# Optimization experiments

Hardware: AMD Instinct MI355X
Metric: run time of the kernel (lower is better)

## Reference

```python
import jax, jax.numpy as jnp
import numpy as np

N_NODES = 50000
N_EDGES = 1600000
HIDDEN = 128
IN_DIM = 3  # x (1) + relative pos (2)


def setup_inputs() -> dict:
    key = jax.random.key(0)
    ks = jax.random.split(key, 5)
    x = jax.random.normal(ks[0], (N_NODES, 1), dtype=jnp.float32)
    pos = jax.random.normal(ks[1], (N_NODES, 2), dtype=jnp.float32)
    # MLP params (Linear(3,128) -> ReLU -> Linear(128,128)), fan-in scaled
    W1 = jax.random.normal(ks[2], (IN_DIM, HIDDEN), dtype=jnp.float32) / np.sqrt(IN_DIM)
    b1 = jnp.zeros((HIDDEN,), dtype=jnp.float32)
    W2 = jax.random.normal(ks[3], (HIDDEN, HIDDEN), dtype=jnp.float32) / np.sqrt(HIDDEN)
    b2 = jnp.zeros((HIDDEN,), dtype=jnp.float32)
    edge_index = jax.random.randint(ks[4], (2, N_EDGES), 0, N_NODES, dtype=jnp.int64)
    return {"x": x, "pos": pos, "W1": W1, "b1": b1, "W2": W2, "b2": b2,
            "edge_index": edge_index}


def reference(x, pos, W1, b1, W2, b2, edge_index):
    # PTConv with aggr='add': per-edge message = nn(cat([x_j, pos_j - pos_i]))
    # then scatter-add into destination node i.
    src = edge_index[0]  # j (neighbor / source)
    dst = edge_index[1]  # i (center / destination)
    msg_in = jnp.concatenate([x[src], pos[src] - pos[dst]], axis=-1)  # [E, 3]
    h = jax.nn.relu(msg_in @ W1 + b1) @ W2 + b2                        # [E, 128]
    out = jax.ops.segment_sum(h, dst, num_segments=x.shape[0])        # [N, 128]
    return out
```

## Files before the change

### kernel.cpp

```cpp
#include <hip/hip_runtime.h>


#define HIDDEN 128
#define BNODES 16
#define BSH 4
#define SUPSH 10
#define CAPA 36864
#define CAPF 768
#define EPBA 1024
#define KSUB 16
#define SThrB 512
#define W2LD 136

typedef float v2f __attribute__((ext_vector_type(2)));
typedef short bf16x8 __attribute__((ext_vector_type(8)));
typedef float f32x4 __attribute__((ext_vector_type(4)));

__device__ __forceinline__ unsigned cvt_pk_bf16(float lo, float hi) {
    unsigned r;
    asm("v_cvt_pk_bf16_f32 %0, %1, %2" : "=v"(r) : "v"(lo), "v"(hi));
    return r;
}

__device__ __forceinline__ unsigned short f2bf(float f) {
    unsigned int u = __float_as_uint(f);
    u += 0x7fffu + ((u >> 16) & 1u);
    return (unsigned short)(u >> 16);
}

__global__ __launch_bounds__(256) void k_histA(const int* __restrict__ dst,
                                               const float* __restrict__ x,
                                               const float* __restrict__ pos,
                                               const float* __restrict__ W2,
                                               int* __restrict__ histA,
                                               float4* __restrict__ xpos,
                                               unsigned short* __restrict__ w2bfT,
                                               int E, int N, int NBLK) {
    __shared__ int h[64];
    int tid = threadIdx.x;
    if (tid < 64) h[tid] = 0;
    int nb = blockIdx.x * 64 + tid;
    if (tid < 64 && nb < N) {
        float2 p = ((const float2*)pos)[nb];
        xpos[nb] = make_float4(x[nb], p.x, p.y, 0.f);
    }
    if (blockIdx.x == gridDim.x - 1) {
        for (int idx = tid; idx < HIDDEN * HIDDEN; idx += 256) {
            int k = idx >> 7, c = idx & 127;
            w2bfT[c * HIDDEN + k] = f2bf(W2[idx]);
        }
    }
    __syncthreads();
    int base = blockIdx.x * EPBA;
    int lim = base + EPBA; if (lim > E) lim = E;
    if (base < lim) {
        int n = lim - base;
        int n4 = ((E & 3) == 0) ? (n >> 2) : 0;
        const int4* d4 = (const int4*)(dst + base);
        for (int i = tid; i < n4; i += 256) {
            int4 d = d4[i];
            atomicAdd(&h[d.x >> SUPSH], 1);
            atomicAdd(&h[d.y >> SUPSH], 1);
            atomicAdd(&h[d.z >> SUPSH], 1);
            atomicAdd(&h[d.w >> SUPSH], 1);
        }
        for (int i = base + (n4 << 2) + tid; i < lim; i += 256)
            atomicAdd(&h[dst[i] >> SUPSH], 1);
    }
    __syncthreads();
    if (tid < 64 && blockIdx.x < NBLK) histA[tid * NBLK + blockIdx.x] = h[tid];
}

__global__ __launch_bounds__(256) void k_scanA(int* __restrict__ histA,
                                               int* __restrict__ bcurA, int NBLK) {
    __shared__ int sums[256];
    int s = blockIdx.x;
    int tid = threadIdx.x;
    int* col = histA + (size_t)s * NBLK;
    int per = (NBLK + 255) >> 8;
    int b0 = tid * per;
    int b1 = b0 + per; if (b1 > NBLK) b1 = NBLK; if (b0 > NBLK) b0 = NBLK;
    int sum = 0;
    for (int b = b0; b < b1; ++b) sum += col[b];
    sums[tid] = sum;
    __syncthreads();
    #pragma unroll
    for (int off = 1; off < 256; off <<= 1) {
        int v = (tid >= off) ? sums[tid - off] : 0;
        __syncthreads();
        sums[tid] += v;
        __syncthreads();
    }
    int run = s * CAPA + ((tid == 0) ? 0 : sums[tid - 1]);
    for (int b = b0; b < b1; ++b) { int t = col[b]; col[b] = run; run += t; }
    if (tid == 255) bcurA[s] = sums[255];
}

__global__ __launch_bounds__(256) void k_placeA(const int* __restrict__ src,
                                                const int* __restrict__ dst,
                                                const int* __restrict__ histA,
                                                unsigned int* __restrict__ pairsA,
                                                int E, int NBLK) {
    __shared__ int h[64];
    __shared__ int hb[64];
    int tid = threadIdx.x;
    if (tid < 64) { hb[tid] = histA[tid * NBLK + blockIdx.x]; h[tid] = 0; }
    __syncthreads();
    int base = blockIdx.x * EPBA;
    int lim = base + EPBA; if (lim > E) lim = E;
    int n = lim - base;
    int n4 = ((E & 3) == 0) ? (n >> 2) : 0;
    const int4* d4 = (const int4*)(dst + base);
    const int4* s4 = (const int4*)(src + base);
#define PUTA(dd, ss) { int sb = (dd) >> SUPSH; int slot = hb[sb] + atomicAdd(&h[sb], 1); \
        if (slot < (sb + 1) * CAPA) pairsA[slot] = ((unsigned)(ss) << SUPSH) | (unsigned)((dd) & 1023); }
    for (int i = tid; i < n4; i += 256) {
        int4 d = d4[i];
        int4 s = s4[i];
        PUTA(d.x, s.x) PUTA(d.y, s.y) PUTA(d.z, s.z) PUTA(d.w, s.w)
    }
    for (int i = base + (n4 << 2) + tid; i < lim; i += 256) {
        int dd = dst[i], ss = src[i];
        PUTA(dd, ss)
    }
#undef PUTA
}

__global__ __launch_bounds__(SThrB) void k_scatB(const int* __restrict__ bcurA,
                                                 const unsigned int* __restrict__ pairsA,
                                                 int* __restrict__ bcurF,
                                                 unsigned int* __restrict__ pairsF,
                                                 int NB) {
    __shared__ int h[64];
    __shared__ int hb[64];
    int tid = threadIdx.x;
    int s = blockIdx.x / KSUB;
    int k = blockIdx.x % KSUB;
    int base0 = s * CAPA;
    int ec = bcurA[s]; if (ec > CAPA) ec = CAPA;
    int slice = (((ec + KSUB - 1) / KSUB) + 3) & ~3;
    int lo = base0 + k * slice;
    int e1 = base0 + ec;
    int hi = lo + slice; if (hi > e1) hi = e1;
    int n = hi - lo; if (n < 0) n = 0;
    int n4 = n >> 2;
    const uint4* p4 = (const uint4*)(pairsA + lo);
    if (tid < 64) h[tid] = 0;
    __syncthreads();
    for (int i = tid; i < n4; i += SThrB) {
        uint4 e = p4[i];
        atomicAdd(&h[(e.x >> BSH) & 63u], 1);
        atomicAdd(&h[(e.y >> BSH) & 63u], 1);
        atomicAdd(&h[(e.z >> BSH) & 63u], 1);
        atomicAdd(&h[(e.w >> BSH) & 63u], 1);
    }
    for (int i = lo + (n4 << 2) + tid; i < hi; i += SThrB)
        atomicAdd(&h[(pairsA[i] >> BSH) & 63u], 1);
    __syncthreads();
    if (tid < 64) {
        int c = h[tid];
        int fb = s * 64 + tid;
        hb[tid] = (c && fb < NB) ? atomicAdd(&bcurF[fb], c) : 0;
        h[tid] = 0;
    }
    __syncthreads();
#define PUTB(ee) { int fbl = (int)(((ee) >> BSH) & 63u); int fb = s * 64 + fbl; \
        int loc = hb[fbl] + atomicAdd(&h[fbl], 1); \
        if (fb < NB && loc < CAPF) pairsF[(size_t)fb * CAPF + loc] = (((ee) >> SUPSH) << BSH) | ((ee) & 15u); }
    for (int i = tid; i < n4; i += SThrB) {
        uint4 e = p4[i];
        PUTB(e.x) PUTB(e.y) PUTB(e.z) PUTB(e.w)
    }
    for (int i = lo + (n4 << 2) + tid; i < hi; i += SThrB) {
        unsigned int e = pairsA[i];
        PUTB(e)
    }
#undef PUTB
}

__global__ __launch_bounds__(256) void k_main(const float4* __restrict__ xpos,
                                              const float* __restrict__ W1,
                                              const float* __restrict__ b1,
                                              const int* __restrict__ bcurF,
                                              const unsigned int* __restrict__ pairs,
                                              float* __restrict__ agg,
                                              int* __restrict__ deg, int N) {
    __shared__ __align__(16) uint2 f_s[CAPF];
    __shared__ int cnt[BNODES];
    __shared__ int offn[BNODES + 1];
    __shared__ int cur[BNODES];

    int tid = threadIdx.x, lane = tid & 63, w = tid >> 6;
    int b = blockIdx.x;
    int n0 = b * BNODES;
    int e0 = b * CAPF;
    int ec = bcurF[b]; if (ec > CAPF) ec = CAPF;

    int c0 = 2 * lane;
    v2f w10 = { W1[c0],              W1[c0 + 1] };
    v2f w11 = { W1[HIDDEN + c0],     W1[HIDDEN + c0 + 1] };
    v2f w12 = { W1[2 * HIDDEN + c0], W1[2 * HIDDEN + c0 + 1] };
    v2f b1v = { b1[c0], b1[c0 + 1] };
    const v2f zero = { 0.f, 0.f };

    if (tid < BNODES) cnt[tid] = 0;
    __syncthreads();
    unsigned int rr0 = 0, rr1 = 0, rr2 = 0;
    if (tid + 0 * 256 < ec) rr0 = pairs[e0 + tid + 0 * 256];
    if (tid + 1 * 256 < ec) rr1 = pairs[e0 + tid + 1 * 256];
    if (tid + 2 * 256 < ec) rr2 = pairs[e0 + tid + 2 * 256];
    if (tid + 0 * 256 < ec) atomicAdd(&cnt[rr0 & 15u], 1);
    if (tid + 1 * 256 < ec) atomicAdd(&cnt[rr1 & 15u], 1);
    if (tid + 2 * 256 < ec) atomicAdd(&cnt[rr2 & 15u], 1);
    __syncthreads();
    if (tid < BNODES) {
        int v = cnt[tid];
        int sc = v;
        #pragma unroll
        for (int d = 1; d < BNODES; d <<= 1) {
            int u = __shfl_up(sc, d);
            if (lane >= d) sc += u;
        }
        offn[tid + 1] = sc;
        if (tid == 0) offn[0] = 0;
        cur[tid] = sc - v;
    }
    __syncthreads();
    #pragma unroll
    for (int q = 0; q < 3; ++q) {
        unsigned int r = q == 0 ? rr0 : q == 1 ? rr1 : rr2;
        if (tid + q * 256 < ec) {
            int j = (int)(r >> BSH);
            int local = (int)(r & 15u);
            float4 f = xpos[j];
            unsigned pk = cvt_pk_bf16(f.y, f.z);
            int p = atomicAdd(&cur[local], 1);
            f_s[p] = make_uint2(pk, __float_as_uint(f.x));
        }
    }
    __syncthreads();
    v2f acc[4];
    int dga[4];
    #pragma unroll
    for (int s = 0; s < 4; ++s) {
        int l = w * 4 + s;
        int node = n0 + l;
        int sb = offn[l], se = offn[l + 1];
        dga[s] = se - sb;
        float4 pi = (node < N) ? xpos[node] : make_float4(0.f, 0.f, 0.f, 0.f);
        v2f t2 = pi.z * w12;
        t2 = pi.y * w11 + t2;
        v2f bb = b1v - t2;
        v2f A = zero;
        #pragma unroll 4
        for (int tt = sb; tt < se; ++tt) {
            uint2 r = f_s[tt];
            float px = __uint_as_float(r.x << 16);
            float py = __uint_as_float(r.x & 0xffff0000u);
            float a  = __uint_as_float(r.y);
            v2f h = a * w10 + bb;
            h = px * w11 + h;
            h = py * w12 + h;
            h = __builtin_elementwise_max(h, zero);
            A += h;
        }
        acc[s] = A;
    }

    #pragma unroll
    for (int s = 0; s < 4; ++s) {
        int l = w * 4 + s;
        int node = n0 + l;
        if (node < N) {
            ((v2f*)&agg[(size_t)node * HIDDEN])[lane] = acc[s];
            if (lane == 0) deg[node] = dga[s];
        }
    }
}

__global__ __launch_bounds__(256) void k_w2(float* __restrict__ agg,
                                            const unsigned short* __restrict__ w2bfT,
                                            const float* __restrict__ b2,
                                            const int* __restrict__ deg, int N) {
    __shared__ unsigned short w2t[HIDDEN * W2LD];
    int tid = threadIdx.x;
    for (int idx = tid; idx < HIDDEN * HIDDEN / 8; idx += 256) {
        int e = idx * 8;
        int c = e >> 7, k0 = e & 127;
        uint4 v = ((const uint4*)w2bfT)[idx];
        *(uint4*)&w2t[c * W2LD + k0] = v;
    }
    __syncthreads();

    int lane = tid & 63, w = tid >> 6;
    int row0 = blockIdx.x * 64 + w * 16;
    if (row0 >= N) return;

    int rA = row0 + (lane & 15);
    int koff = (lane >> 4) * 8;
    bool okA = rA < N;

    bf16x8 a[4];
    #pragma unroll
    for (int k0 = 0; k0 < 4; ++k0) {
        float4 fa = {0.f,0.f,0.f,0.f}, fb = {0.f,0.f,0.f,0.f};
        if (okA) {
            const float4* p = (const float4*)&agg[(size_t)rA * HIDDEN + k0 * 32 + koff];
            fa = p[0]; fb = p[1];
        }
        union { uint4 u; bf16x8 v; } cv;
        cv.u.x = cvt_pk_bf16(fa.x, fa.y);
        cv.u.y = cvt_pk_bf16(fa.z, fa.w);
        cv.u.z = cvt_pk_bf16(fb.x, fb.y);
        cv.u.w = cvt_pk_bf16(fb.z, fb.w);
        a[k0] = cv.v;
    }

    f32x4 acc[8];
    #pragma unroll
    for (int ct = 0; ct < 8; ++ct) acc[ct] = (f32x4){0.f,0.f,0.f,0.f};

    #pragma unroll
    for (int ct = 0; ct < 8; ++ct) {
        int col = ct * 16 + (lane & 15);
        #pragma unroll
        for (int k0 = 0; k0 < 4; ++k0) {
            bf16x8 bfrag = *(const bf16x8*)&w2t[col * W2LD + k0 * 32 + koff];
            acc[ct] = __builtin_amdgcn_mfma_f32_16x16x32_bf16(a[k0], bfrag, acc[ct], 0, 0, 0);
        }
    }

    int mbase = row0 + (lane >> 4) * 4;
    float dg[4];
    #pragma unroll
    for (int i = 0; i < 4; ++i) dg[i] = (mbase + i < N) ? (float)deg[mbase + i] : 0.f;

    #pragma unroll
    for (int ct = 0; ct < 8; ++ct) {
        int col = ct * 16 + (lane & 15);
        float b2c = b2[col];
        #pragma unroll
        for (int i = 0; i < 4; ++i) {
            int r = mbase + i;
            if (r < N) agg[(size_t)r * HIDDEN + col] = acc[ct][i] + dg[i] * b2c;
        }
    }
}

extern "C" void kernel_launch(void* const* d_in, const int* in_sizes, int n_in,
                              void* d_out, int out_size, void* d_ws, size_t ws_size,
                              hipStream_t stream) {
    const float* x   = (const float*)d_in[0];
    const float* pos = (const float*)d_in[1];
    const float* W1  = (const float*)d_in[2];
    const float* b1  = (const float*)d_in[3];
    const float* W2  = (const float*)d_in[4];
    const float* b2  = (const float*)d_in[5];
    const int*   ei  = (const int*)d_in[6];

    int N = in_sizes[0];
    int E = in_sizes[6] / 2;
    const int* src = ei;
    const int* dst = ei + E;
    float* out = (float*)d_out;

    int NB   = (N + BNODES - 1) / BNODES;
    int NSUP = (N + 1023) >> SUPSH;
    int NBLK = (E + EPBA - 1) / EPBA;

    int* bcurA = (int*)d_ws;
    int* bcurF = bcurA + 64;
    int* deg   = bcurF + NB;
    int* histA = deg + N;
    unsigned short* w2bfT = (unsigned short*)(histA + (size_t)64 * NBLK);
    float4* xpos = (float4*)(w2bfT + HIDDEN * HIDDEN);
    unsigned int* pairsA = (unsigned int*)(xpos + ((N + 63) & ~63));
    unsigned int* pairsF = pairsA + (size_t)NSUP * CAPA;

    int nblk_nodes = (N + 63) / 64;
    int gribsA = NBLK > nblk_nodes ? NBLK : nblk_nodes;

    hipMemsetAsync(bcurF, 0, (size_t)NB * sizeof(int), stream);
    k_histA<<<gribsA, 256, 0, stream>>>(dst, x, pos, W2, histA, xpos, w2bfT, E, N, NBLK);
    k_scanA<<<64, 256, 0, stream>>>(histA, bcurA, NBLK);
    k_placeA<<<NBLK, 256, 0, stream>>>(src, dst, histA, pairsA, E, NBLK);
    k_scatB<<<NSUP * KSUB, SThrB, 0, stream>>>(bcurA, pairsA, bcurF, pairsF, NB);
    k_main<<<NB, 256, 0, stream>>>(xpos, W1, b1, bcurF, pairsF, out, deg, N);
    k_w2<<<(N + 63) / 64, 256, 0, stream>>>(out, w2bfT, b2, deg, N);
}
```

Measured before the change: 106.2 us.

## Gather node features during bucket scatter and store packed 8-byte edge records

The xpos gather and bf16 packing move from k_main into k_scatB, which now writes 8-byte records holding packed pos and x, with the local node id stuffed into x's low mantissa bits. k_main then only counts and scatters these records into shared memory, with no dependent global gather. In exchange the pairsF traffic doubles and x loses 4 mantissa bits. CAPF drops to 640 and EPBA doubles to 2048, which changes per-bucket capacity and the histogram block count.

```diff
diff --git a/kernel.cpp b/kernel.cpp
--- a/kernel.cpp
+++ b/kernel.cpp
@@ -6,8 +6,8 @@
 #define BSH 4
 #define SUPSH 10
 #define CAPA 36864
-#define CAPF 768
-#define EPBA 1024
+#define CAPF 640
+#define EPBA 2048
 #define KSUB 16
 #define SThrB 512
 #define W2LD 136
@@ -128,8 +128,9 @@
 
 __global__ __launch_bounds__(SThrB) void k_scatB(const int* __restrict__ bcurA,
                                                  const unsigned int* __restrict__ pairsA,
+                                                 const float4* __restrict__ xpos,
                                                  int* __restrict__ bcurF,
-                                                 unsigned int* __restrict__ pairsF,
+                                                 uint2* __restrict__ pairsF,
                                                  int NB) {
     __shared__ int h[64];
     __shared__ int hb[64];
@@ -166,7 +167,11 @@
     __syncthreads();
 #define PUTB(ee) { int fbl = (int)(((ee) >> BSH) & 63u); int fb = s * 64 + fbl; \
         int loc = hb[fbl] + atomicAdd(&h[fbl], 1); \
-        if (fb < NB && loc < CAPF) pairsF[(size_t)fb * CAPF + loc] = (((ee) >> SUPSH) << BSH) | ((ee) & 15u); }
+        if (fb < NB && loc < CAPF) { \
+            float4 f = xpos[(ee) >> SUPSH]; \
+            unsigned pk = cvt_pk_bf16(f.y, f.z); \
+            unsigned aw = (__float_as_uint(f.x) & ~15u) | ((ee) & 15u); \
+            pairsF[(size_t)fb * CAPF + loc] = make_uint2(pk, aw); } }
     for (int i = tid; i < n4; i += SThrB) {
         uint4 e = p4[i];
         PUTB(e.x) PUTB(e.y) PUTB(e.z) PUTB(e.w)
@@ -182,7 +187,7 @@
                                               const float* __restrict__ W1,
                                               const float* __restrict__ b1,
                                               const int* __restrict__ bcurF,
-                                              const unsigned int* __restrict__ pairs,
+                                              const uint2* __restrict__ pairs,
                                               float* __restrict__ agg,
                                               int* __restrict__ deg, int N) {
     __shared__ __align__(16) uint2 f_s[CAPF];
@@ -193,7 +198,7 @@
     int tid = threadIdx.x, lane = tid & 63, w = tid >> 6;
     int b = blockIdx.x;
     int n0 = b * BNODES;
-    int e0 = b * CAPF;
+    size_t e0 = (size_t)b * CAPF;
     int ec = bcurF[b]; if (ec > CAPF) ec = CAPF;
 
     int c0 = 2 * lane;
@@ -205,13 +210,13 @@
 
     if (tid < BNODES) cnt[tid] = 0;
     __syncthreads();
-    unsigned int rr0 = 0, rr1 = 0, rr2 = 0;
+    uint2 rr0 = {0,0}, rr1 = {0,0}, rr2 = {0,0};
     if (tid + 0 * 256 < ec) rr0 = pairs[e0 + tid + 0 * 256];
     if (tid + 1 * 256 < ec) rr1 = pairs[e0 + tid + 1 * 256];
     if (tid + 2 * 256 < ec) rr2 = pairs[e0 + tid + 2 * 256];
-    if (tid + 0 * 256 < ec) atomicAdd(&cnt[rr0 & 15u], 1);
-    if (tid + 1 * 256 < ec) atomicAdd(&cnt[rr1 & 15u], 1);
-    if (tid + 2 * 256 < ec) atomicAdd(&cnt[rr2 & 15u], 1);
+    if (tid + 0 * 256 < ec) atomicAdd(&cnt[rr0.y & 15u], 1);
+    if (tid + 1 * 256 < ec) atomicAdd(&cnt[rr1.y & 15u], 1);
+    if (tid + 2 * 256 < ec) atomicAdd(&cnt[rr2.y & 15u], 1);
     __syncthreads();
     if (tid < BNODES) {
         int v = cnt[tid];
@@ -228,14 +233,10 @@
     __syncthreads();
     #pragma unroll
     for (int q = 0; q < 3; ++q) {
-        unsigned int r = q == 0 ? rr0 : q == 1 ? rr1 : rr2;
+        uint2 r = q == 0 ? rr0 : q == 1 ? rr1 : rr2;
         if (tid + q * 256 < ec) {
-            int j = (int)(r >> BSH);
-            int local = (int)(r & 15u);
-            float4 f = xpos[j];
-            unsigned pk = cvt_pk_bf16(f.y, f.z);
-            int p = atomicAdd(&cur[local], 1);
-            f_s[p] = make_uint2(pk, __float_as_uint(f.x));
+            int p = atomicAdd(&cur[r.y & 15u], 1);
+            f_s[p] = r;
         }
     }
     __syncthreads();
@@ -375,7 +376,7 @@
     unsigned short* w2bfT = (unsigned short*)(histA + (size_t)64 * NBLK);
     float4* xpos = (float4*)(w2bfT + HIDDEN * HIDDEN);
     unsigned int* pairsA = (unsigned int*)(xpos + ((N + 63) & ~63));
-    unsigned int* pairsF = pairsA + (size_t)NSUP * CAPA;
+    uint2* pairsF = (uint2*)(pairsA + (size_t)NSUP * CAPA);
 
     int nblk_nodes = (N + 63) / 64;
     int gribsA = NBLK > nblk_nodes ? NBLK : nblk_nodes;
@@ -384,7 +385,7 @@
     k_histA<<<gribsA, 256, 0, stream>>>(dst, x, pos, W2, histA, xpos, w2bfT, E, N, NBLK);
     k_scanA<<<64, 256, 0, stream>>>(histA, bcurA, NBLK);
     k_placeA<<<NBLK, 256, 0, stream>>>(src, dst, histA, pairsA, E, NBLK);
-    k_scatB<<<NSUP * KSUB, SThrB, 0, stream>>>(bcurA, pairsA, bcurF, pairsF, NB);
+    k_scatB<<<NSUP * KSUB, SThrB, 0, stream>>>(bcurA, pairsA, xpos, bcurF, pairsF, NB);
     k_main<<<NB, 256, 0, stream>>>(xpos, W1, b1, bcurF, pairsF, out, deg, N);
     k_w2<<<(N + 63) / 64, 256, 0, stream>>>(out, w2bfT, b2, deg, N);
 }
```

After: 108.5 us. 2.2% more time.

## Fuse W2 MFMA projection into k_main via LDS-staged aggregates

Applied to the files above, without the earlier changes.

Removes the separate k_w2 kernel. Each k_main block now keeps its 16 nodes' aggregated first-layer activations and degrees in LDS and applies the bf16 MFMA W2 projection plus the deg*b2 bias directly. That avoids writing the fp32 intermediate to global memory, reading it back, and one kernel launch. In exchange, every wave in a block runs the same 16-row MFMA, and W2 fragments come straight from global/L2 for each block instead of a shared LDS copy. EPBA is also doubled, which changes the block granularity of the edge histogram and placement stages.

```diff
diff --git a/kernel.cpp b/kernel.cpp
--- a/kernel.cpp
+++ b/kernel.cpp
@@ -7,10 +7,10 @@
 #define SUPSH 10
 #define CAPA 36864
 #define CAPF 768
-#define EPBA 1024
+#define EPBA 2048
 #define KSUB 16
 #define SThrB 512
-#define W2LD 136
+#define ALDS 132
 
 typedef float v2f __attribute__((ext_vector_type(2)));
 typedef short bf16x8 __attribute__((ext_vector_type(8)));
@@ -181,11 +181,14 @@
 __global__ __launch_bounds__(256) void k_main(const float4* __restrict__ xpos,
                                               const float* __restrict__ W1,
                                               const float* __restrict__ b1,
+                                              const unsigned short* __restrict__ w2bfT,
+                                              const float* __restrict__ b2,
                                               const int* __restrict__ bcurF,
                                               const unsigned int* __restrict__ pairs,
-                                              float* __restrict__ agg,
-                                              int* __restrict__ deg, int N) {
+                                              float* __restrict__ out, int N) {
     __shared__ __align__(16) uint2 f_s[CAPF];
+    __shared__ __align__(16) float accLds[BNODES][ALDS];
+    __shared__ float degS[BNODES];
     __shared__ int cnt[BNODES];
     __shared__ int offn[BNODES + 1];
     __shared__ int cur[BNODES];
@@ -239,14 +242,11 @@
         }
     }
     __syncthreads();
-    v2f acc[4];
-    int dga[4];
     #pragma unroll
     for (int s = 0; s < 4; ++s) {
         int l = w * 4 + s;
         int node = n0 + l;
         int sb = offn[l], se = offn[l + 1];
-        dga[s] = se - sb;
         float4 pi = (node < N) ? xpos[node] : make_float4(0.f, 0.f, 0.f, 0.f);
         v2f t2 = pi.z * w12;
         t2 = pi.y * w11 + t2;
@@ -264,85 +264,54 @@
             h = __builtin_elementwise_max(h, zero);
             A += h;
         }
-        acc[s] = A;
-    }
-
-    #pragma unroll
-    for (int s = 0; s < 4; ++s) {
-        int l = w * 4 + s;
-        int node = n0 + l;
-        if (node < N) {
-            ((v2f*)&agg[(size_t)node * HIDDEN])[lane] = acc[s];
-            if (lane == 0) deg[node] = dga[s];
-        }
-    }
-}
-
-__global__ __launch_bounds__(256) void k_w2(float* __restrict__ agg,
-                                            const unsigned short* __restrict__ w2bfT,
-                                            const float* __restrict__ b2,
-                                            const int* __restrict__ deg, int N) {
-    __shared__ unsigned short w2t[HIDDEN * W2LD];
-    int tid = threadIdx.x;
-    for (int idx = tid; idx < HIDDEN * HIDDEN / 8; idx += 256) {
-        int e = idx * 8;
-        int c = e >> 7, k0 = e & 127;
-        uint4 v = ((const uint4*)w2bfT)[idx];
-        *(uint4*)&w2t[c * W2LD + k0] = v;
-    }
-    __syncthreads();
-
-    int lane = tid & 63, w = tid >> 6;
-    int row0 = blockIdx.x * 64 + w * 16;
-    if (row0 >= N) return;
-
-    int rA = row0 + (lane & 15);
+        ((v2f*)&accLds[l][0])[lane] = A;
+        if (lane == 0) degS[l] = (float)(se - sb);
+    }
+    __syncthreads();
+
+    int m = lane & 15;
     int koff = (lane >> 4) * 8;
-    bool okA = rA < N;
-
-    bf16x8 a[4];
+    bf16x8 afr[4];
     #pragma unroll
     for (int k0 = 0; k0 < 4; ++k0) {
-        float4 fa = {0.f,0.f,0.f,0.f}, fb = {0.f,0.f,0.f,0.f};
-        if (okA) {
-            const float4* p = (const float4*)&agg[(size_t)rA * HIDDEN + k0 * 32 + koff];
-            fa = p[0]; fb = p[1];
-        }
+        const float* p = &accLds[m][k0 * 32 + koff];
+        float4 fa = *(const float4*)p;
+        float4 fb = *(const float4*)(p + 4);
         union { uint4 u; bf16x8 v; } cv;
         cv.u.x = cvt_pk_bf16(fa.x, fa.y);
         cv.u.y = cvt_pk_bf16(fa.z, fa.w);
         cv.u.z = cvt_pk_bf16(fb.x, fb.y);
         cv.u.w = cvt_pk_bf16(fb.z, fb.w);
-        a[k0] = cv.v;
-    }
-
-    f32x4 acc[8];
-    #pragma unroll
-    for (int ct = 0; ct < 8; ++ct) acc[ct] = (f32x4){0.f,0.f,0.f,0.f};
+        afr[k0] = cv.v;
+    }
+
+    f32x4 macc[8];
+    #pragma unroll
+    for (int ct = 0; ct < 8; ++ct) macc[ct] = (f32x4){0.f, 0.f, 0.f, 0.f};
 
     #pragma unroll
     for (int ct = 0; ct < 8; ++ct) {
-        int col = ct * 16 + (lane & 15);
+        int col = ct * 16 + m;
         #pragma unroll
         for (int k0 = 0; k0 < 4; ++k0) {
-            bf16x8 bfrag = *(const bf16x8*)&w2t[col * W2LD + k0 * 32 + koff];
-            acc[ct] = __builtin_amdgcn_mfma_f32_16x16x32_bf16(a[k0], bfrag, acc[ct], 0, 0, 0);
-        }
-    }
-
-    int mbase = row0 + (lane >> 4) * 4;
+            bf16x8 bfrag = *(const bf16x8*)&w2bfT[col * HIDDEN + k0 * 32 + koff];
+            macc[ct] = __builtin_amdgcn_mfma_f32_16x16x32_bf16(afr[k0], bfrag, macc[ct], 0, 0, 0);
+        }
+    }
+
+    int mbase = (lane >> 4) * 4;
     float dg[4];
     #pragma unroll
-    for (int i = 0; i < 4; ++i) dg[i] = (mbase + i < N) ? (float)deg[mbase + i] : 0.f;
+    for (int i = 0; i < 4; ++i) dg[i] = degS[mbase + i];
 
     #pragma unroll
     for (int ct = 0; ct < 8; ++ct) {
-        int col = ct * 16 + (lane & 15);
+        int col = ct * 16 + m;
         float b2c = b2[col];
         #pragma unroll
         for (int i = 0; i < 4; ++i) {
-            int r = mbase + i;
-            if (r < N) agg[(size_t)r * HIDDEN + col] = acc[ct][i] + dg[i] * b2c;
+            int node = n0 + mbase + i;
+            if (node < N) out[(size_t)node * HIDDEN + col] = macc[ct][i] + dg[i] * b2c;
         }
     }
 }
@@ -370,8 +339,7 @@
 
     int* bcurA = (int*)d_ws;
     int* bcurF = bcurA + 64;
-    int* deg   = bcurF + NB;
-    int* histA = deg + N;
+    int* histA = bcurF + NB;
     unsigned short* w2bfT = (unsigned short*)(histA + (size_t)64 * NBLK);
     float4* xpos = (float4*)(w2bfT + HIDDEN * HIDDEN);
     unsigned int* pairsA = (unsigned int*)(xpos + ((N + 63) & ~63));
@@ -385,6 +353,5 @@
     k_scanA<<<64, 256, 0, stream>>>(histA, bcurA, NBLK);
     k_placeA<<<NBLK, 256, 0, stream>>>(src, dst, histA, pairsA, E, NBLK);
     k_scatB<<<NSUP * KSUB, SThrB, 0, stream>>>(bcurA, pairsA, bcurF, pairsF, NB);
-    k_main<<<NB, 256, 0, stream>>>(xpos, W1, b1, bcurF, pairsF, out, deg, N);
-    k_w2<<<(N + 63) / 64, 256, 0, stream>>>(out, w2bfT, b2, deg, N);
-}
+    k_main<<<NB, 256, 0, stream>>>(xpos, W1, b1, w2bfT, b2, bcurF, pairsF, out, N);
+}
```

New measurement: 133.0 us. +25.2%, slower.
